# Optimization experiments

Hardware: AMD Instinct MI355X
Metric: run time of the kernel (lower is better)

Reference implementation:

```python
import jax, jax.numpy as jnp
import numpy as np

S, B, H, K = 4096, 1, 2048, 2  # seq_len, batch (forced to 1 by the view()), hidden_dim, conv kernel
EMBED = K * K                  # embed_dim must equal kernel_size**2
THRESHOLD = 0.0


def setup_inputs() -> dict:
    key = jax.random.key(0)
    k0, k1, k2 = jax.random.split(key, 3)
    inputs = jax.random.normal(k0, (S, B, EMBED), dtype=jnp.float32)
    # ConvFilter params: Conv2d(1,1,K) on a KxK patch == dot with flattened kernel + bias
    conv_w = jax.random.normal(k1, (EMBED,), dtype=jnp.float32) * 0.5
    conv_b = jnp.zeros((1,), dtype=jnp.float32)
    # Four gate Linears (1+H -> H) stacked column-wise into one (1+H, 4H) matmul
    # order: forget | input | update | output  (same math as 4 separate nn.Linear)
    w_gates = (jax.random.normal(k2, (1 + H, 4 * H), dtype=jnp.float32)
               / np.sqrt(1.0 + H)).astype(jnp.float32)
    b_gates = jnp.zeros((4 * H,), dtype=jnp.float32)
    return {"inputs": inputs, "conv_w": conv_w, "conv_b": conv_b,
            "w_gates": w_gates, "b_gates": b_gates}


def reference(inputs, conv_w, conv_b, w_gates, b_gates):
    S_, B_, _ = inputs.shape
    H_ = w_gates.shape[1] // 4

    # Conv preprocess (vectorized over all timesteps): each (K,K) token patch
    # -> scalar sigmoid(conv(x) - threshold), then mean over the per-step batch
    # (batch==1, so the mean is the value itself, matching torch's .mean()).
    conv_scalar = jax.nn.sigmoid(inputs @ conv_w + conv_b[0] - THRESHOLD)  # (S, B)
    conv_scalar = jnp.mean(conv_scalar, axis=1, keepdims=True)             # (S, 1)
    conv_out = jnp.broadcast_to(conv_scalar[:, :, None], (S_, B_, 1))      # (S, B, 1)

    hx0 = jnp.zeros((B_, H_), dtype=inputs.dtype)
    cx0 = jnp.zeros((B_, H_), dtype=inputs.dtype)

    def step(carry, c_t):
        hx, cx = carry
        combined = jnp.concatenate([c_t, hx], axis=1)        # (B, 1+H)
        gates = combined @ w_gates + b_gates                  # (B, 4H) fused 4-gate GEMM
        f, i, g, o = jnp.split(gates, 4, axis=1)
        f = jax.nn.sigmoid(f)
        i = jax.nn.sigmoid(i)
        g = jnp.tanh(g)
        o = jax.nn.sigmoid(o)
        cx = f * cx + i * g
        hx = o * jnp.tanh(cx)
        return (hx, cx), hx

    (hx, cx), stacked = jax.lax.scan(step, (hx0, cx0), conv_out)
    return stacked, hx, cx
```

## Files before the change

### kernel.cpp

```cpp
#include <hip/hip_runtime.h>
#include <math.h>

#define S_LEN 4096
#define HID   2048
#define NBLK  256
#define NTHR  512
#define RSTRIDE (2*HID+16)

typedef unsigned long long u64;
typedef float v2f __attribute__((ext_vector_type(2)));
typedef unsigned int v4u __attribute__((ext_vector_type(4)));


__device__ __forceinline__ float fsig(float x) {
    return 1.0f / (1.0f + __expf(-x));
}
__device__ __forceinline__ float ftanh(float x) {
    float e = __expf(2.0f * fabsf(x));
    float r = 1.0f - 2.0f / (e + 1.0f);
    return copysignf(r, x);
}

__device__ __forceinline__ void ld16x2(const u64* pa, const u64* pb, v4u& A, v4u& B) {
    asm volatile("global_load_dwordx4 %0, %2, off sc0 sc1\n\t"
                 "global_load_dwordx4 %1, %3, off sc0 sc1\n\t"
                 "s_waitcnt vmcnt(0)"
                 : "=&v"(A), "=&v"(B) : "v"(pa), "v"(pb) : "memory");
}
__device__ __forceinline__ v4u ld16(const u64* p) {
    v4u r;
    asm volatile("global_load_dwordx4 %0, %1, off sc0 sc1\n\t"
                 "s_waitcnt vmcnt(0)"
                 : "=&v"(r) : "v"(p) : "memory");
    return r;
}

__global__ __launch_bounds__(NTHR, 2)
void qlstm_persistent(const float* __restrict__ inp,
                      const float* __restrict__ conv_w,
                      const float* __restrict__ conv_b,
                      const float* __restrict__ Wg,
                      const float* __restrict__ bg,
                      float* __restrict__ out,
                      float* __restrict__ ws,
                      int nmask)
{
    const int b   = blockIdx.x;
    const int tid = threadIdx.x;
    const int l   = tid & 63;
    const int wv  = tid >> 6;

    u64* tb = (u64*)ws;

    __shared__ __align__(16) float hx_lds[HID];
    __shared__ __align__(16) float conv_lds[S_LEN];
    __shared__ float gates_lds[32];

    {
        const float cw0 = conv_w[0], cw1 = conv_w[1], cw2 = conv_w[2], cw3 = conv_w[3];
        const float cb  = conv_b[0];
        for (int g = tid; g < S_LEN; g += NTHR) {
            float4 x = ((const float4*)inp)[g];
            conv_lds[g] = fsig(x.x*cw0 + x.y*cw1 + x.z*cw2 + x.w*cw3 + cb);
        }
    }

    int jcol[4];
    #pragma unroll
    for (int c = 0; c < 4; ++c) {
        int cgi  = 4*wv + c;
        jcol[c]  = ((cgi >> 3) << 11) + (b * 8 + (cgi & 7));
    }

    float cw_reg[4], cb_reg[4];
    {
        int u8 = b * 8 + (tid & 7);
        #pragma unroll
        for (int c = 0; c < 4; ++c) {
            cw_reg[c] = Wg[(c << 11) + u8];
            cb_reg[c] = bg[(c << 11) + u8];
        }
    }

    v2f wreg2[4][16];
    #pragma unroll
    for (int j = 0; j < 8; ++j)
        #pragma unroll
        for (int p = 0; p < 2; ++p) {
            const float* r0 = Wg + (size_t)(1 + 4*l + 256*j + 2*p) * 8192;
            const float* r1 = r0 + 8192;
            #pragma unroll
            for (int c = 0; c < 4; ++c)
                wreg2[c][2*j + p] = (v2f){ r0[jcol[c]], r1[jcol[c]] };
        }

    float cx = 0.0f;
    const int unit = b * 8 + (tid & 7);
    const int reg  = b & nmask;

    if (tid < 8) {
        u64 pub = (u64)1 << 32;
        for (int r = 0; r <= nmask; ++r)
            __hip_atomic_store(&tb[(size_t)r*RSTRIDE + unit], pub,
                               __ATOMIC_RELAXED, __HIP_MEMORY_SCOPE_AGENT);
    }

    const int pair0 = (wv << 8) + 2*l;

    for (int t = 0; t < S_LEN; ++t) {
        const unsigned want = (unsigned)(t + 1);
        const u64* base = tb + (size_t)reg*RSTRIDE + (size_t)(t & 1)*HID;
        u64*       nbuf = tb + (size_t)((t + 1) & 1)*HID;
        const u64* p0 = base + pair0;
        const u64* p1 = base + pair0 + 128;

        v4u A, B;
        ld16x2(p0, p1, A, B);
        unsigned pend = 3u;
        for (;;) {
            if ((pend & 1u) && A.y == want && A.w == want) pend &= ~1u;
            if ((pend & 2u) && B.y == want && B.w == want) pend &= ~2u;
            if (!pend) break;
            if (pend == 3u)      ld16x2(p0, p1, A, B);
            else if (pend & 1u)  A = ld16(p0);
            else                 B = ld16(p1);
        }
        ((float2*)hx_lds)[(wv << 7) + l] =
            (float2){ __uint_as_float(A.x), __uint_as_float(A.z) };
        ((float2*)hx_lds)[(wv << 7) + 64 + l] =
            (float2){ __uint_as_float(B.x), __uint_as_float(B.z) };
        __syncthreads();

        const float4* hl = (const float4*)hx_lds;
        v2f a0 = {0.f, 0.f}, a1 = {0.f, 0.f}, a2 = {0.f, 0.f}, a3 = {0.f, 0.f};
        #pragma unroll
        for (int j = 0; j < 8; ++j) {
            float4 h = hl[l + 64*j];
            v2f h01 = { h.x, h.y };
            v2f h23 = { h.z, h.w };
            a0 = __builtin_elementwise_fma(h01, wreg2[0][2*j  ], a0);
            a1 = __builtin_elementwise_fma(h01, wreg2[1][2*j  ], a1);
            a2 = __builtin_elementwise_fma(h01, wreg2[2][2*j  ], a2);
            a3 = __builtin_elementwise_fma(h01, wreg2[3][2*j  ], a3);
            a0 = __builtin_elementwise_fma(h23, wreg2[0][2*j+1], a0);
            a1 = __builtin_elementwise_fma(h23, wreg2[1][2*j+1], a1);
            a2 = __builtin_elementwise_fma(h23, wreg2[2][2*j+1], a2);
            a3 = __builtin_elementwise_fma(h23, wreg2[3][2*j+1], a3);
        }
        float acc0 = a0.x + a0.y;
        float acc1 = a1.x + a1.y;
        float acc2 = a2.x + a2.y;
        float acc3 = a3.x + a3.y;
        #pragma unroll
        for (int off = 32; off; off >>= 1) {
            acc0 += __shfl_down(acc0, off, 64);
            acc1 += __shfl_down(acc1, off, 64);
            acc2 += __shfl_down(acc2, off, 64);
            acc3 += __shfl_down(acc3, off, 64);
        }
        if (l == 0) {
            gates_lds[4*wv + 0] = acc0;
            gates_lds[4*wv + 1] = acc1;
            gates_lds[4*wv + 2] = acc2;
            gates_lds[4*wv + 3] = acc3;
        }
        __syncthreads();

        if (tid < 8) {
            float ct = conv_lds[t];
            float f  = fsig (gates_lds[tid]      + ct*cw_reg[0] + cb_reg[0]);
            float ii = fsig (gates_lds[8 + tid]  + ct*cw_reg[1] + cb_reg[1]);
            float gv = ftanh(gates_lds[16 + tid] + ct*cw_reg[2] + cb_reg[2]);
            float o  = fsig (gates_lds[24 + tid] + ct*cw_reg[3] + cb_reg[3]);
            cx = f * cx + ii * gv;
            float hx = o * ftanh(cx);
            u64 pub = ((u64)(unsigned)(t + 2) << 32) | (u64)__float_as_uint(hx);
            for (int r = 0; r <= nmask; ++r)
                __hip_atomic_store(&nbuf[(size_t)r*RSTRIDE + unit], pub,
                                   __ATOMIC_RELAXED, __HIP_MEMORY_SCOPE_AGENT);
            out[(size_t)t * HID + unit] = hx;
            if (t == S_LEN - 1) {
                out[(size_t)S_LEN * HID + unit]       = hx;
                out[(size_t)S_LEN * HID + HID + unit] = cx;
            }
        }
    }
}

extern "C" void kernel_launch(void* const* d_in, const int* in_sizes, int n_in,
                              void* d_out, int out_size, void* d_ws, size_t ws_size,
                              hipStream_t stream) {
    const float* inp    = (const float*)d_in[0];
    const float* conv_w = (const float*)d_in[1];
    const float* conv_b = (const float*)d_in[2];
    const float* Wg     = (const float*)d_in[3];
    const float* bg     = (const float*)d_in[4];
    float* out = (float*)d_out;
    float* ws  = (float*)d_ws;

    size_t rbytes = (size_t)RSTRIDE * 8;
    int nrep = 1;
    while (nrep < 8 && (size_t)(nrep * 2) * rbytes <= ws_size) nrep *= 2;
    int nmask = nrep - 1;

    void* args[] = {(void*)&inp, (void*)&conv_w, (void*)&conv_b,
                    (void*)&Wg, (void*)&bg, (void*)&out, (void*)&ws, (void*)&nmask};
    hipLaunchCooperativeKernel((void*)qlstm_persistent,
                               dim3(NBLK), dim3(NTHR), args, 0, stream);
}
```

Before: 13.57 ms.

## Pipeline flag polling with two in-flight loads and drop replicated publish buffers

The per-step spin-wait on the hidden-state buffer now keeps two pairs of 16-byte loads in flight. It waits on the older pair with a partial vmcnt and reissues the next pair straight away, instead of a blocking load-then-check loop. The publish scheme is also simplified: each unit writes one copy of its tagged hidden value, where before it wrote up to eight replicated regions that different blocks read from. This is meant to cut poll round-trip latency and publish store traffic on the serial critical path. The cost is that all 256 blocks now poll the same cache lines, which can increase contention.

New measurement: 13.38 ms. Within noise of the previous version (-1.4%).

```diff
diff --git a/kernel.cpp b/kernel.cpp
--- a/kernel.cpp
+++ b/kernel.cpp
@@ -5,7 +5,6 @@
 #define HID   2048
 #define NBLK  256
 #define NTHR  512
-#define RSTRIDE (2*HID+16)
 
 typedef unsigned long long u64;
 typedef float v2f __attribute__((ext_vector_type(2)));
@@ -21,19 +20,13 @@
     return copysignf(r, x);
 }
 
-__device__ __forceinline__ void ld16x2(const u64* pa, const u64* pb, v4u& A, v4u& B) {
-    asm volatile("global_load_dwordx4 %0, %2, off sc0 sc1\n\t"
-                 "global_load_dwordx4 %1, %3, off sc0 sc1\n\t"
-                 "s_waitcnt vmcnt(0)"
-                 : "=&v"(A), "=&v"(B) : "v"(pa), "v"(pb) : "memory");
-}
-__device__ __forceinline__ v4u ld16(const u64* p) {
-    v4u r;
-    asm volatile("global_load_dwordx4 %0, %1, off sc0 sc1\n\t"
-                 "s_waitcnt vmcnt(0)"
-                 : "=&v"(r) : "v"(p) : "memory");
-    return r;
-}
+#define POLL_ISSUE(Ra, Rb)                                         \
+    asm volatile("global_load_dwordx4 %0, %2, off sc0 sc1\n\t"     \
+                 "global_load_dwordx4 %1, %3, off sc0 sc1"         \
+                 : "=&v"(Ra), "=&v"(Rb) : "v"(p0), "v"(p1) : "memory")
+
+#define POLL_WAIT2(Ra, Rb)                                         \
+    asm volatile("s_waitcnt vmcnt(2)" : "+v"(Ra), "+v"(Rb))
 
 __global__ __launch_bounds__(NTHR, 2)
 void qlstm_persistent(const float* __restrict__ inp,
@@ -42,15 +35,15 @@
                       const float* __restrict__ Wg,
                       const float* __restrict__ bg,
                       float* __restrict__ out,
-                      float* __restrict__ ws,
-                      int nmask)
+                      float* __restrict__ ws)
 {
     const int b   = blockIdx.x;
     const int tid = threadIdx.x;
     const int l   = tid & 63;
     const int wv  = tid >> 6;
 
-    u64* tb = (u64*)ws;
+    u64* tb0 = (u64*)ws;
+    u64* tb1 = tb0 + HID + 16;
 
     __shared__ __align__(16) float hx_lds[HID];
     __shared__ __align__(16) float conv_lds[S_LEN];
@@ -96,39 +89,43 @@
 
     float cx = 0.0f;
     const int unit = b * 8 + (tid & 7);
-    const int reg  = b & nmask;
-
-    if (tid < 8) {
-        u64 pub = (u64)1 << 32;
-        for (int r = 0; r <= nmask; ++r)
-            __hip_atomic_store(&tb[(size_t)r*RSTRIDE + unit], pub,
-                               __ATOMIC_RELAXED, __HIP_MEMORY_SCOPE_AGENT);
-    }
-
-    const int pair0 = (wv << 8) + 2*l;
+
+    if (tid < 8)
+        __hip_atomic_store(&tb0[unit], (u64)1 << 32,
+                           __ATOMIC_RELAXED, __HIP_MEMORY_SCOPE_AGENT);
+
+    const int pairoff = (wv << 8) + 2*l;
 
     for (int t = 0; t < S_LEN; ++t) {
         const unsigned want = (unsigned)(t + 1);
-        const u64* base = tb + (size_t)reg*RSTRIDE + (size_t)(t & 1)*HID;
-        u64*       nbuf = tb + (size_t)((t + 1) & 1)*HID;
-        const u64* p0 = base + pair0;
-        const u64* p1 = base + pair0 + 128;
-
-        v4u A, B;
-        ld16x2(p0, p1, A, B);
-        unsigned pend = 3u;
+        const u64* base = (t & 1) ? tb1 : tb0;
+        u64*       nbuf = (t & 1) ? tb0 : tb1;
+        const u64* p0 = base + pairoff;
+        const u64* p1 = base + pairoff + 128;
+
+        v4u A0, A1, B0, B1;
+        POLL_ISSUE(A0, A1);
+        POLL_ISSUE(B0, B1);
+        unsigned r0, r1, r2, r3;
         for (;;) {
-            if ((pend & 1u) && A.y == want && A.w == want) pend &= ~1u;
-            if ((pend & 2u) && B.y == want && B.w == want) pend &= ~2u;
-            if (!pend) break;
-            if (pend == 3u)      ld16x2(p0, p1, A, B);
-            else if (pend & 1u)  A = ld16(p0);
-            else                 B = ld16(p1);
-        }
+            POLL_WAIT2(A0, A1);
+            if (A0.y == want && A0.w == want && A1.y == want && A1.w == want) {
+                r0 = A0.x; r1 = A0.z; r2 = A1.x; r3 = A1.z; break;
+            }
+            POLL_ISSUE(A0, A1);
+            POLL_WAIT2(B0, B1);
+            if (B0.y == want && B0.w == want && B1.y == want && B1.w == want) {
+                r0 = B0.x; r1 = B0.z; r2 = B1.x; r3 = B1.z; break;
+            }
+            POLL_ISSUE(B0, B1);
+        }
+        asm volatile("s_waitcnt vmcnt(0)"
+                     : "+v"(A0), "+v"(A1), "+v"(B0), "+v"(B1) :: "memory");
+
         ((float2*)hx_lds)[(wv << 7) + l] =
-            (float2){ __uint_as_float(A.x), __uint_as_float(A.z) };
+            (float2){ __uint_as_float(r0), __uint_as_float(r1) };
         ((float2*)hx_lds)[(wv << 7) + 64 + l] =
-            (float2){ __uint_as_float(B.x), __uint_as_float(B.z) };
+            (float2){ __uint_as_float(r2), __uint_as_float(r3) };
         __syncthreads();
 
         const float4* hl = (const float4*)hx_lds;
@@ -174,10 +171,9 @@
             float o  = fsig (gates_lds[24 + tid] + ct*cw_reg[3] + cb_reg[3]);
             cx = f * cx + ii * gv;
             float hx = o * ftanh(cx);
-            u64 pub = ((u64)(unsigned)(t + 2) << 32) | (u64)__float_as_uint(hx);
-            for (int r = 0; r <= nmask; ++r)
-                __hip_atomic_store(&nbuf[(size_t)r*RSTRIDE + unit], pub,
-                                   __ATOMIC_RELAXED, __HIP_MEMORY_SCOPE_AGENT);
+            __hip_atomic_store(&nbuf[unit],
+                               ((u64)(unsigned)(t + 2) << 32) | (u64)__float_as_uint(hx),
+                               __ATOMIC_RELAXED, __HIP_MEMORY_SCOPE_AGENT);
             out[(size_t)t * HID + unit] = hx;
             if (t == S_LEN - 1) {
                 out[(size_t)S_LEN * HID + unit]       = hx;
@@ -198,13 +194,9 @@
     float* out = (float*)d_out;
     float* ws  = (float*)d_ws;
 
-    size_t rbytes = (size_t)RSTRIDE * 8;
-    int nrep = 1;
-    while (nrep < 8 && (size_t)(nrep * 2) * rbytes <= ws_size) nrep *= 2;
-    int nmask = nrep - 1;
 
     void* args[] = {(void*)&inp, (void*)&conv_w, (void*)&conv_b,
-                    (void*)&Wg, (void*)&bg, (void*)&out, (void*)&ws, (void*)&nmask};
+                    (void*)&Wg, (void*)&bg, (void*)&out, (void*)&ws};
     hipLaunchCooperativeKernel((void*)qlstm_persistent,
                                dim3(NBLK), dim3(NTHR), args, 0, stream);
 }
```
